# Kernel tuning notes

Measured on AMD Instinct MI355X. Metric: run time of the kernel, lower is better.

## Reference

```python
import jax, jax.numpy as jnp
import numpy as np


def log_g(x):
    # log of g(x) = where(x>=0, x+0.5, sigmoid(x))
    return jnp.where(x >= 0, jnp.log(jnp.maximum(x, 0.0) + 0.5), -jax.nn.softplus(-x))


def setup_inputs() -> dict:
    key = jax.random.key(0)
    k1, k2 = jax.random.split(key)
    B, S, D = 8, 8192, 512
    x = jax.random.normal(k1, (B, S, D), dtype=jnp.float32)
    # to_hidden_and_gate weight: [2*D, D] (orthogonal init in torch; gaussian ok for reference)
    W = jax.random.normal(k2, (2 * D, D), dtype=jnp.float32) / np.sqrt(D)
    return {"x": x, "W": W}


def reference(x, W):
    # x: [B, S, D], W: [2D, D]
    hg = jnp.einsum('bsd,ed->bse', x, W)  # [B, S, 2D]
    D = x.shape[-1]
    hidden, gate = hg[..., :D], hg[..., D:]

    # log-domain minGRU (Heinsen associative scan)
    log_coeffs = -jax.nn.softplus(gate)            # log(1 - z)
    log_z = -jax.nn.softplus(-gate)                # log(z)
    log_values = log_z + log_g(hidden)             # log(z * g(h~))

    a_star = jnp.cumsum(log_coeffs, axis=1)
    log_h = a_star + jax.lax.cumlogsumexp(log_values - a_star, axis=1)
    out = jnp.exp(log_h)                           # [B, S, D]

    next_prev_hidden = out[:, -1:]
    return out, next_prev_hidden
```

## Files before the change

### kernel.cpp

```cpp
#include <hip/hip_runtime.h>
#include <hip/hip_bf16.h>
#include <stdint.h>

typedef float f32x4 __attribute__((ext_vector_type(4)));
typedef __bf16 bf16x8 __attribute__((ext_vector_type(8)));
typedef unsigned short ushort8 __attribute__((ext_vector_type(8)));

#define NB 8
#define NS 8192
#define ND 512
#define NM (NB * NS)
#define NK 512

__device__ __forceinline__ unsigned short f2bf(float f) {
  unsigned u = __float_as_uint(f);
  u += 0x7FFFu + ((u >> 16) & 1u);
  return (unsigned short)(u >> 16);
}

__global__ __launch_bounds__(256) void cvt_bf16(const float* __restrict__ src,
                                                unsigned short* __restrict__ dst,
                                                int n8) {
  int i = blockIdx.x * 256 + threadIdx.x;
  if (i >= n8) return;
  const float4* s = reinterpret_cast<const float4*>(src + (size_t)i * 8);
  float4 v0 = s[0], v1 = s[1];
  ushort8 o;
  o[0] = f2bf(v0.x); o[1] = f2bf(v0.y); o[2] = f2bf(v0.z); o[3] = f2bf(v0.w);
  o[4] = f2bf(v1.x); o[5] = f2bf(v1.y); o[6] = f2bf(v1.z); o[7] = f2bf(v1.w);
  *reinterpret_cast<ushort8*>(dst + (size_t)i * 8) = o;
}

__global__ __launch_bounds__(512, 2) void gemm_ab(const unsigned short* __restrict__ xb,
                                                  const unsigned short* __restrict__ wb,
                                                  uint32_t* __restrict__ pk,
                                                  float* __restrict__ aggA,
                                                  float* __restrict__ aggB) {
  __shared__ __align__(16) char lds[2 * 65536];

  const int tid = threadIdx.x;
  const int w = tid >> 6;
  const int lane = tid & 63;
  const int wm = w >> 2;
  const int wn = w & 3;
  const int orig = blockIdx.x;
  const int wg = (orig & 7) * 128 + (orig >> 3);
  const int mblk = wg >> 2;
  const int nblk = wg & 3;
  const int m0 = mblk * 256;
  const int n0 = nblk * 128;

  const int lrow = lane >> 3;
  const int lcol = (((lane & 7) ^ lrow) * 8);

  const unsigned short* pA[4];
  const unsigned short* pB[4];
#pragma unroll
  for (int g = 0; g < 4; ++g) {
    int row = g * 64 + w * 8 + lrow;
    pA[g] = xb + (size_t)(m0 + row) * NK + lcol;
    int e = (row < 128) ? (n0 + row) : (384 + n0 + row);
    pB[g] = wb + (size_t)e * NK + lcol;
  }

  auto stage = [&](int buf, int kt) {
    char* base = lds + buf * 65536;
    const int ko = kt << 6;
#pragma unroll
    for (int g = 0; g < 4; ++g) {
      __builtin_amdgcn_global_load_lds(
          (const __attribute__((address_space(1))) void*)(pA[g] + ko),
          (__attribute__((address_space(3))) void*)(base + g * 8192 + w * 1024),
          16, 0, 0);
      __builtin_amdgcn_global_load_lds(
          (const __attribute__((address_space(1))) void*)(pB[g] + ko),
          (__attribute__((address_space(3))) void*)(base + 32768 + g * 8192 + w * 1024),
          16, 0, 0);
    }
  };

  const int fr = lane & 15;
  const int kg = lane >> 4;

  f32x4 acc[8][4];
#pragma unroll
  for (int i = 0; i < 8; ++i)
#pragma unroll
    for (int j = 0; j < 4; ++j) acc[i][j] = (f32x4)0.0f;

  stage(0, 0);
  __syncthreads();

#pragma unroll 1
  for (int kt = 0; kt < 8; ++kt) {
    const int cur = kt & 1;
    if (kt < 7) stage(cur ^ 1, kt + 1);

    const char* ldsA = lds + cur * 65536;
    const char* ldsB = ldsA + 32768;
#pragma unroll
    for (int kk = 0; kk < 64; kk += 32) {
      bf16x8 af[8], bfr[4];
#pragma unroll
      for (int i = 0; i < 8; ++i) {
        int rowA = wm * 128 + i * 16 + fr;
        int sa = (kk * 2 + kg * 16) ^ ((rowA & 7) << 4);
        af[i] = *reinterpret_cast<const bf16x8*>(ldsA + rowA * 128 + sa);
      }
#pragma unroll
      for (int n = 0; n < 4; ++n) {
        int rowB = ((n < 2) ? (wn * 32 + n * 16) : (128 + wn * 32 + (n - 2) * 16)) + fr;
        int sb = (kk * 2 + kg * 16) ^ ((rowB & 7) << 4);
        bfr[n] = *reinterpret_cast<const bf16x8*>(ldsB + rowB * 128 + sb);
      }
#pragma unroll
      for (int i = 0; i < 8; ++i)
#pragma unroll
        for (int j = 0; j < 4; ++j)
          acc[i][j] = __builtin_amdgcn_mfma_f32_16x16x32_bf16(af[i], bfr[j], acc[i][j], 0, 0, 0);
    }
    __syncthreads();
  }

  const float LOG2E = 1.44269504f;
#pragma unroll
  for (int n = 0; n < 2; ++n) {
    const int ch = wn * 32 + n * 16 + fr;
    float Am[8], Bm[8];
#pragma unroll
    for (int m = 0; m < 8; ++m) {
      float As = 1.0f, Bs = 0.0f;
#pragma unroll
      for (int r = 0; r < 4; ++r) {
        float hid = acc[m][n][r];
        float gat = acc[m][n + 2][r];
        float ex1 = __builtin_amdgcn_exp2f(gat * LOG2E);
        float a = __builtin_amdgcn_rcpf(1.0f + ex1);
        float z = 1.0f - a;
        float ex2 = __builtin_amdgcn_exp2f(-hid * LOG2E);
        float gn = __builtin_amdgcn_rcpf(1.0f + ex2);
        float g = (hid >= 0.0f) ? (hid + 0.5f) : gn;
        float bb = z * g;
        int row = wm * 128 + 16 * m + 4 * kg + r;
        pk[(size_t)(m0 + row) * ND + n0 + ch] =
            ((uint32_t)f2bf(bb) << 16) | (uint32_t)f2bf(a);
        Bs = fmaf(a, Bs, bb);
        As *= a;
      }
      Am[m] = As; Bm[m] = Bs;
    }
#pragma unroll
    for (int m = 0; m < 8; ++m) {
      float pA_ = __shfl_xor(Am[m], 16);
      float pB_ = __shfl_xor(Bm[m], 16);
      Bm[m] = (kg & 1) ? fmaf(Am[m], pB_, Bm[m]) : fmaf(pA_, Bm[m], pB_);
      Am[m] *= pA_;
      pA_ = __shfl_xor(Am[m], 32);
      pB_ = __shfl_xor(Bm[m], 32);
      Bm[m] = (kg & 2) ? fmaf(Am[m], pB_, Bm[m]) : fmaf(pA_, Bm[m], pB_);
      Am[m] *= pA_;
    }
    float As = Am[0], Bs = Bm[0];
#pragma unroll
    for (int m = 1; m < 8; ++m) { Bs = fmaf(Am[m], Bs, Bm[m]); As *= Am[m]; }
    if (kg == 0) {
      size_t o = (size_t)(mblk * 2 + wm) * ND + n0 + ch;
      aggA[o] = As;
      aggB[o] = Bs;
    }
  }
}

__global__ __launch_bounds__(256) void scan_pass2(const uint32_t* __restrict__ pk,
                                                  const float* __restrict__ aggA,
                                                  const float* __restrict__ aggB,
                                                  float* __restrict__ out,
                                                  float* __restrict__ nextp) {
  int bid = blockIdx.x;
  int b = bid >> 6;
  int c = bid & 63;
  int d2 = threadIdx.x;

  float h0 = 0.0f, h1 = 0.0f;
  for (int cc = 0; cc < c; ++cc) {
    int o = (b * 64 + cc) * ND + d2 * 2;
    float2 Aa = *reinterpret_cast<const float2*>(&aggA[o]);
    float2 Bb = *reinterpret_cast<const float2*>(&aggB[o]);
    h0 = fmaf(Aa.x, h0, Bb.x);
    h1 = fmaf(Aa.y, h1, Bb.y);
  }
  size_t base = (size_t)(b * NS + c * 128) * ND + d2 * 2;
#pragma unroll 4
  for (int t = 0; t < 128; ++t) {
    size_t idx = base + (size_t)t * ND;
    uint2 v = *reinterpret_cast<const uint2*>(pk + idx);
    float a0 = __uint_as_float(v.x << 16);
    float b0 = __uint_as_float(v.x & 0xffff0000u);
    float a1 = __uint_as_float(v.y << 16);
    float b1 = __uint_as_float(v.y & 0xffff0000u);
    h0 = fmaf(a0, h0, b0);
    h1 = fmaf(a1, h1, b1);
    *reinterpret_cast<float2*>(&out[idx]) = make_float2(h0, h1);
  }
  if (c == 63) {
    *reinterpret_cast<float2*>(&nextp[b * ND + d2 * 2]) = make_float2(h0, h1);
  }
}

extern "C" void kernel_launch(void* const* d_in, const int* in_sizes, int n_in,
                              void* d_out, int out_size, void* d_ws, size_t ws_size,
                              hipStream_t stream) {
  const float* x = (const float*)d_in[0];
  const float* W = (const float*)d_in[1];
  float* out = (float*)d_out;

  char* ws = (char*)d_ws;
  unsigned short* xb  = (unsigned short*)ws;
  unsigned short* wbf = (unsigned short*)(ws + (size_t)64 * 1024 * 1024);
  uint32_t* pk = (uint32_t*)(ws + (size_t)65 * 1024 * 1024);
  float* aggA = (float*)(ws + (size_t)193 * 1024 * 1024);
  float* aggB = (float*)(ws + (size_t)194 * 1024 * 1024);
  float* nextp = out + (size_t)NM * ND;

  cvt_bf16<<<16384, 256, 0, stream>>>(x, xb, (NM * NK) / 8);
  cvt_bf16<<<256, 256, 0, stream>>>(W, wbf, (1024 * NK) / 8);
  gemm_ab<<<1024, 512, 0, stream>>>(xb, wbf, pk, aggA, aggB);
  scan_pass2<<<512, 256, 0, stream>>>(pk, aggA, aggB, out, nextp);
}
```

Before: 225.1 us.

## Triple-buffer GEMM K-loop with 32-wide K tiles and explicit waitcnt scheduling

Restructures the GEMM main loop from double-buffered 64-wide K tiles to triple-buffered 32-wide K tiles, fully unrolled over 16 steps. Loads for step k+2 are issued while the current step computes, and waits use explicit vmcnt/lgkmcnt with sched barriers and setprio around the MFMA block. It also changes the LDS swizzle for the 64-byte rows and drops the 2-blocks-per-CU launch bound. The aim is to hide global-load latency better, at the cost of twice as many barriers and possible occupancy and register-pressure changes.

```diff
diff --git a/kernel.cpp b/kernel.cpp
--- a/kernel.cpp
+++ b/kernel.cpp
@@ -31,12 +31,12 @@
   *reinterpret_cast<ushort8*>(dst + (size_t)i * 8) = o;
 }
 
-__global__ __launch_bounds__(512, 2) void gemm_ab(const unsigned short* __restrict__ xb,
-                                                  const unsigned short* __restrict__ wb,
-                                                  uint32_t* __restrict__ pk,
-                                                  float* __restrict__ aggA,
-                                                  float* __restrict__ aggB) {
-  __shared__ __align__(16) char lds[2 * 65536];
+__global__ __launch_bounds__(512) void gemm_ab(const unsigned short* __restrict__ xb,
+                                               const unsigned short* __restrict__ wb,
+                                               uint32_t* __restrict__ pk,
+                                               float* __restrict__ aggA,
+                                               float* __restrict__ aggB) {
+  __shared__ __align__(16) char lds[3 * 32768];
 
   const int tid = threadIdx.x;
   const int w = tid >> 6;
@@ -50,37 +50,20 @@
   const int m0 = mblk * 256;
   const int n0 = nblk * 128;
 
-  const int lrow = lane >> 3;
-  const int lcol = (((lane & 7) ^ lrow) * 8);
-
-  const unsigned short* pA[4];
-  const unsigned short* pB[4];
-#pragma unroll
-  for (int g = 0; g < 4; ++g) {
-    int row = g * 64 + w * 8 + lrow;
-    pA[g] = xb + (size_t)(m0 + row) * NK + lcol;
+  const int cg = ((lane & 3) ^ ((lane >> 3) & 3)) << 3;
+  const unsigned short* pA2[2];
+  const unsigned short* pB2[2];
+#pragma unroll
+  for (int g = 0; g < 2; ++g) {
+    int row = (g * 8 + w) * 16 + (lane >> 2);
+    pA2[g] = xb + (size_t)(m0 + row) * NK + cg;
     int e = (row < 128) ? (n0 + row) : (384 + n0 + row);
-    pB[g] = wb + (size_t)e * NK + lcol;
-  }
-
-  auto stage = [&](int buf, int kt) {
-    char* base = lds + buf * 65536;
-    const int ko = kt << 6;
-#pragma unroll
-    for (int g = 0; g < 4; ++g) {
-      __builtin_amdgcn_global_load_lds(
-          (const __attribute__((address_space(1))) void*)(pA[g] + ko),
-          (__attribute__((address_space(3))) void*)(base + g * 8192 + w * 1024),
-          16, 0, 0);
-      __builtin_amdgcn_global_load_lds(
-          (const __attribute__((address_space(1))) void*)(pB[g] + ko),
-          (__attribute__((address_space(3))) void*)(base + 32768 + g * 8192 + w * 1024),
-          16, 0, 0);
-    }
-  };
+    pB2[g] = wb + (size_t)e * NK + cg;
+  }
 
   const int fr = lane & 15;
   const int kg = lane >> 4;
+  const int rsw = ((kg ^ ((fr >> 1) & 3)) << 4);
 
   f32x4 acc[8][4];
 #pragma unroll
@@ -88,39 +71,94 @@
 #pragma unroll
     for (int j = 0; j < 4; ++j) acc[i][j] = (f32x4)0.0f;
 
-  stage(0, 0);
-  __syncthreads();
-
-#pragma unroll 1
-  for (int kt = 0; kt < 8; ++kt) {
-    const int cur = kt & 1;
-    if (kt < 7) stage(cur ^ 1, kt + 1);
-
-    const char* ldsA = lds + cur * 65536;
-    const char* ldsB = ldsA + 32768;
-#pragma unroll
-    for (int kk = 0; kk < 64; kk += 32) {
-      bf16x8 af[8], bfr[4];
-#pragma unroll
-      for (int i = 0; i < 8; ++i) {
-        int rowA = wm * 128 + i * 16 + fr;
-        int sa = (kk * 2 + kg * 16) ^ ((rowA & 7) << 4);
-        af[i] = *reinterpret_cast<const bf16x8*>(ldsA + rowA * 128 + sa);
-      }
-#pragma unroll
-      for (int n = 0; n < 4; ++n) {
-        int rowB = ((n < 2) ? (wn * 32 + n * 16) : (128 + wn * 32 + (n - 2) * 16)) + fr;
-        int sb = (kk * 2 + kg * 16) ^ ((rowB & 7) << 4);
-        bfr[n] = *reinterpret_cast<const bf16x8*>(ldsB + rowB * 128 + sb);
-      }
-#pragma unroll
-      for (int i = 0; i < 8; ++i)
-#pragma unroll
-        for (int j = 0; j < 4; ++j)
-          acc[i][j] = __builtin_amdgcn_mfma_f32_16x16x32_bf16(af[i], bfr[j], acc[i][j], 0, 0, 0);
-    }
-    __syncthreads();
-  }
+  bf16x8 af[8], bfr[4];
+
+#define GLD(SRC, DSTOFF)                                                      \
+  __builtin_amdgcn_global_load_lds(                                           \
+      (const __attribute__((address_space(1))) void*)(SRC),                   \
+      (__attribute__((address_space(3))) void*)(lds + (DSTOFF)), 16, 0, 0)
+
+#define STAGE(S, KT)                                                          \
+  {                                                                           \
+    GLD(pA2[0] + (KT) * 32, (S) * 32768 + (0 * 8 + w) * 1024);                \
+    GLD(pA2[1] + (KT) * 32, (S) * 32768 + (1 * 8 + w) * 1024);                \
+    GLD(pB2[0] + (KT) * 32, (S) * 32768 + 16384 + (0 * 8 + w) * 1024);        \
+    GLD(pB2[1] + (KT) * 32, (S) * 32768 + 16384 + (1 * 8 + w) * 1024);        \
+  }
+
+#define READF(C)                                                              \
+  {                                                                           \
+    const char* ldsA_ = lds + (C) * 32768;                                    \
+    const char* ldsB_ = ldsA_ + 16384;                                        \
+    _Pragma("unroll")                                                         \
+    for (int i = 0; i < 8; ++i) {                                             \
+      int rowA = wm * 128 + i * 16 + fr;                                      \
+      af[i] = *reinterpret_cast<const bf16x8*>(ldsA_ + rowA * 64 + rsw);      \
+    }                                                                         \
+    _Pragma("unroll")                                                         \
+    for (int n = 0; n < 4; ++n) {                                             \
+      int rowB = ((n < 2) ? (wn * 32 + n * 16) : (128 + wn * 32 + (n - 2) * 16)) + fr; \
+      bfr[n] = *reinterpret_cast<const bf16x8*>(ldsB_ + rowB * 64 + rsw);     \
+    }                                                                         \
+  }
+
+#define MFMA32()                                                              \
+  {                                                                           \
+    _Pragma("unroll")                                                         \
+    for (int i = 0; i < 8; ++i)                                               \
+      _Pragma("unroll")                                                       \
+      for (int j = 0; j < 4; ++j)                                             \
+        acc[i][j] = __builtin_amdgcn_mfma_f32_16x16x32_bf16(af[i], bfr[j],    \
+                                                            acc[i][j], 0, 0, 0); \
+  }
+
+#define BAR() __builtin_amdgcn_s_barrier()
+#define SB0() __builtin_amdgcn_sched_barrier(0)
+#define LGKM0() asm volatile("s_waitcnt lgkmcnt(0)" ::: "memory")
+#define VMC(N) asm volatile("s_waitcnt vmcnt(" #N ")" ::: "memory")
+
+#define ITER(KT, C, S, DO, WMODE)                                             \
+  {                                                                           \
+    READF(C);                                                                 \
+    if (DO) STAGE(S, (KT) + 2);                                               \
+    BAR(); LGKM0(); SB0();                                                    \
+    __builtin_amdgcn_s_setprio(1); MFMA32(); __builtin_amdgcn_s_setprio(0);   \
+    if (WMODE == 1) { VMC(4); SB0(); }                                        \
+    if (WMODE == 2) { VMC(0); SB0(); }                                        \
+    BAR();                                                                    \
+  }
+
+  STAGE(0, 0);
+  STAGE(1, 1);
+  VMC(4); SB0();
+  BAR();
+
+  ITER(0,  0, 2, 1, 1);
+  ITER(1,  1, 0, 1, 1);
+  ITER(2,  2, 1, 1, 1);
+  ITER(3,  0, 2, 1, 1);
+  ITER(4,  1, 0, 1, 1);
+  ITER(5,  2, 1, 1, 1);
+  ITER(6,  0, 2, 1, 1);
+  ITER(7,  1, 0, 1, 1);
+  ITER(8,  2, 1, 1, 1);
+  ITER(9,  0, 2, 1, 1);
+  ITER(10, 1, 0, 1, 1);
+  ITER(11, 2, 1, 1, 1);
+  ITER(12, 0, 2, 1, 1);
+  ITER(13, 1, 0, 1, 1);
+  ITER(14, 2, 1, 0, 2);
+  ITER(15, 0, 2, 0, 0);
+
+#undef ITER
+#undef GLD
+#undef STAGE
+#undef READF
+#undef MFMA32
+#undef BAR
+#undef SB0
+#undef LGKM0
+#undef VMC
 
   const float LOG2E = 1.44269504f;
 #pragma unroll
```

New measurement: 227.6 us. Within noise of the previous version (+1.1%).

## Fuse x fp32-to-bf16 conversion into GEMM by staging fp32 A tiles in LDS

Applied to the files above, without the earlier changes.

Drops the separate x conversion pass, which reads 128MB of fp32 and writes 64MB of bf16. The GEMM now loads fp32 x tiles straight into LDS in K-chunks of 32, converts them to bf16 with v_cvt_pk_bf16_f32 after the LDS read, and double-buffers B at half the rate. This removes a full round trip of x through memory. The cost is twice the A bytes moved through LDS per MFMA, more K iterations and barriers, and the loss of the 2-blocks-per-CU launch bound.

```diff
diff --git a/kernel.cpp b/kernel.cpp
--- a/kernel.cpp
+++ b/kernel.cpp
@@ -16,6 +16,12 @@
   unsigned u = __float_as_uint(f);
   u += 0x7FFFu + ((u >> 16) & 1u);
   return (unsigned short)(u >> 16);
+}
+
+__device__ __forceinline__ uint32_t cvtpk(float lo, float hi) {
+  uint32_t r;
+  asm("v_cvt_pk_bf16_f32 %0, %1, %2" : "=v"(r) : "v"(lo), "v"(hi));
+  return r;
 }
 
 __global__ __launch_bounds__(256) void cvt_bf16(const float* __restrict__ src,
@@ -31,12 +37,12 @@
   *reinterpret_cast<ushort8*>(dst + (size_t)i * 8) = o;
 }
 
-__global__ __launch_bounds__(512, 2) void gemm_ab(const unsigned short* __restrict__ xb,
-                                                  const unsigned short* __restrict__ wb,
-                                                  uint32_t* __restrict__ pk,
-                                                  float* __restrict__ aggA,
-                                                  float* __restrict__ aggB) {
-  __shared__ __align__(16) char lds[2 * 65536];
+__global__ __launch_bounds__(512) void gemm_ab(const float* __restrict__ x,
+                                               const unsigned short* __restrict__ wb,
+                                               uint32_t* __restrict__ pk,
+                                               float* __restrict__ aggA,
+                                               float* __restrict__ aggB) {
+  __shared__ __align__(16) char lds[131072];
 
   const int tid = threadIdx.x;
   const int w = tid >> 6;
@@ -51,32 +57,41 @@
   const int n0 = nblk * 128;
 
   const int lrow = lane >> 3;
-  const int lcol = (((lane & 7) ^ lrow) * 8);
-
-  const unsigned short* pA[4];
-  const unsigned short* pB[4];
+  const int aSrc = (((lane & 7) ^ lrow) << 2);
+  const float* pAf[4];
+#pragma unroll
+  for (int g = 0; g < 4; ++g) {
+    int row = (g * 8 + w) * 8 + lrow;
+    pAf[g] = x + (size_t)(m0 + row) * NK + aSrc;
+  }
+  const int bSrc = (((lane & 7) ^ lrow) << 3);
+  const unsigned short* pBf[4];
 #pragma unroll
   for (int g = 0; g < 4; ++g) {
     int row = g * 64 + w * 8 + lrow;
-    pA[g] = xb + (size_t)(m0 + row) * NK + lcol;
     int e = (row < 128) ? (n0 + row) : (384 + n0 + row);
-    pB[g] = wb + (size_t)e * NK + lcol;
-  }
-
-  auto stage = [&](int buf, int kt) {
-    char* base = lds + buf * 65536;
-    const int ko = kt << 6;
-#pragma unroll
-    for (int g = 0; g < 4; ++g) {
+    pBf[g] = wb + (size_t)e * NK + bSrc;
+  }
+
+  auto stageA = [&](int buf, int kt) {
+    char* base = lds + buf * 32768;
+    const int ko = kt << 5;
+#pragma unroll
+    for (int g = 0; g < 4; ++g)
       __builtin_amdgcn_global_load_lds(
-          (const __attribute__((address_space(1))) void*)(pA[g] + ko),
+          (const __attribute__((address_space(1))) void*)(pAf[g] + ko),
+          (__attribute__((address_space(3))) void*)(base + (g * 8 + w) * 1024),
+          16, 0, 0);
+  };
+  auto stageB = [&](int buf, int pair) {
+    char* base = lds + 65536 + buf * 32768;
+    const int ko = pair << 6;
+#pragma unroll
+    for (int g = 0; g < 4; ++g)
+      __builtin_amdgcn_global_load_lds(
+          (const __attribute__((address_space(1))) void*)(pBf[g] + ko),
           (__attribute__((address_space(3))) void*)(base + g * 8192 + w * 1024),
           16, 0, 0);
-      __builtin_amdgcn_global_load_lds(
-          (const __attribute__((address_space(1))) void*)(pB[g] + ko),
-          (__attribute__((address_space(3))) void*)(base + 32768 + g * 8192 + w * 1024),
-          16, 0, 0);
-    }
   };
 
   const int fr = lane & 15;
@@ -88,36 +103,43 @@
 #pragma unroll
     for (int j = 0; j < 4; ++j) acc[i][j] = (f32x4)0.0f;
 
-  stage(0, 0);
+  stageA(0, 0);
+  stageB(0, 0);
   __syncthreads();
 
 #pragma unroll 1
-  for (int kt = 0; kt < 8; ++kt) {
+  for (int kt = 0; kt < 16; ++kt) {
     const int cur = kt & 1;
-    if (kt < 7) stage(cur ^ 1, kt + 1);
-
-    const char* ldsA = lds + cur * 65536;
-    const char* ldsB = ldsA + 32768;
-#pragma unroll
-    for (int kk = 0; kk < 64; kk += 32) {
-      bf16x8 af[8], bfr[4];
-#pragma unroll
-      for (int i = 0; i < 8; ++i) {
-        int rowA = wm * 128 + i * 16 + fr;
-        int sa = (kk * 2 + kg * 16) ^ ((rowA & 7) << 4);
-        af[i] = *reinterpret_cast<const bf16x8*>(ldsA + rowA * 128 + sa);
-      }
-#pragma unroll
-      for (int n = 0; n < 4; ++n) {
-        int rowB = ((n < 2) ? (wn * 32 + n * 16) : (128 + wn * 32 + (n - 2) * 16)) + fr;
-        int sb = (kk * 2 + kg * 16) ^ ((rowB & 7) << 4);
-        bfr[n] = *reinterpret_cast<const bf16x8*>(ldsB + rowB * 128 + sb);
-      }
-#pragma unroll
-      for (int i = 0; i < 8; ++i)
-#pragma unroll
-        for (int j = 0; j < 4; ++j)
-          acc[i][j] = __builtin_amdgcn_mfma_f32_16x16x32_bf16(af[i], bfr[j], acc[i][j], 0, 0, 0);
+    const int bp = (kt >> 1) & 1;
+    if (kt < 15) stageA(cur ^ 1, kt + 1);
+    if ((kt & 1) == 0 && kt < 14) stageB(bp ^ 1, (kt >> 1) + 1);
+
+    const char* ldsA = lds + cur * 32768;
+    const char* ldsB = lds + 65536 + bp * 32768;
+    const int kk = (kt & 1) * 32;
+    bf16x8 bfr[4];
+#pragma unroll
+    for (int n = 0; n < 4; ++n) {
+      int rowB = ((n < 2) ? (wn * 32 + n * 16) : (128 + wn * 32 + (n - 2) * 16)) + fr;
+      int sb = (kk * 2 + kg * 16) ^ ((rowB & 7) << 4);
+      bfr[n] = *reinterpret_cast<const bf16x8*>(ldsB + rowB * 128 + sb);
+    }
+#pragma unroll
+    for (int i = 0; i < 8; ++i) {
+      int rowA = wm * 128 + i * 16 + fr;
+      int s0 = (((2 * kg) ^ (fr & 7)) << 4);
+      int s1 = (((2 * kg + 1) ^ (fr & 7)) << 4);
+      f32x4 q0 = *reinterpret_cast<const f32x4*>(ldsA + rowA * 128 + s0);
+      f32x4 q1 = *reinterpret_cast<const f32x4*>(ldsA + rowA * 128 + s1);
+      uint4 u;
+      u.x = cvtpk(q0[0], q0[1]);
+      u.y = cvtpk(q0[2], q0[3]);
+      u.z = cvtpk(q1[0], q1[1]);
+      u.w = cvtpk(q1[2], q1[3]);
+      bf16x8 af = *reinterpret_cast<bf16x8*>(&u);
+#pragma unroll
+      for (int j = 0; j < 4; ++j)
+        acc[i][j] = __builtin_amdgcn_mfma_f32_16x16x32_bf16(af, bfr[j], acc[i][j], 0, 0, 0);
     }
     __syncthreads();
   }
@@ -215,15 +237,13 @@
   float* out = (float*)d_out;
 
   char* ws = (char*)d_ws;
-  unsigned short* xb  = (unsigned short*)ws;
-  unsigned short* wbf = (unsigned short*)(ws + (size_t)64 * 1024 * 1024);
-  uint32_t* pk = (uint32_t*)(ws + (size_t)65 * 1024 * 1024);
-  float* aggA = (float*)(ws + (size_t)193 * 1024 * 1024);
-  float* aggB = (float*)(ws + (size_t)194 * 1024 * 1024);
+  uint32_t* pk = (uint32_t*)ws;
+  unsigned short* wbf = (unsigned short*)(ws + (size_t)128 * 1024 * 1024);
+  float* aggA = (float*)(ws + (size_t)129 * 1024 * 1024);
+  float* aggB = (float*)(ws + (size_t)130 * 1024 * 1024);
   float* nextp = out + (size_t)NM * ND;
 
-  cvt_bf16<<<16384, 256, 0, stream>>>(x, xb, (NM * NK) / 8);
   cvt_bf16<<<256, 256, 0, stream>>>(W, wbf, (1024 * NK) / 8);
-  gemm_ab<<<1024, 512, 0, stream>>>(xb, wbf, pk, aggA, aggB);
+  gemm_ab<<<1024, 512, 0, stream>>>(x, wbf, pk, aggA, aggB);
   scan_pass2<<<512, 256, 0, stream>>>(pk, aggA, aggB, out, nextp);
 }
```

New measurement: 197.6 us, median of 2. -12.2%, faster.
